# Kernel optimization log

Hardware: AMD Instinct MI355X
Metric: run time of the kernel (lower is better)

Reference implementation:

```python
import jax, jax.numpy as jnp
import numpy as np

EPS_LN = 1e-5
EPS_BN = 1e-5
NUM_HEADS = 8


def _gelu(x):
    return jax.nn.gelu(x, approximate=False)


def _ln(x, w, b):
    # LayerNorm over last (channel) dim, eps=1e-5 (torch default)
    mu = jnp.mean(x, axis=-1, keepdims=True)
    var = jnp.mean((x - mu) ** 2, axis=-1, keepdims=True)
    return (x - mu) / jnp.sqrt(var + EPS_LN) * w + b


def _bn(x, g, b):
    # eval-mode BatchNorm2d on NCHW with running_mean=0, running_var=1
    scale = g * (1.0 + EPS_BN) ** -0.5
    return x * scale[None, :, None, None] + b[None, :, None, None]


def _conv1x1(x, w):
    # x: [B,C,H,W], w: [O,C]
    return jnp.einsum('bchw,oc->bohw', x, w)


def _unfold3(x, r):
    # nn.Unfold(kernel=3, dilation=r, padding=r): gather 3x3 dilated neighborhoods
    B, C, H, W = x.shape
    xp = jnp.pad(x, ((0, 0), (0, 0), (r, r), (r, r)))
    pats = [xp[:, :, i * r:i * r + H, j * r:j * r + W] for i in range(3) for j in range(3)]
    return jnp.stack(pats, axis=2)  # [B,C,9,H,W]


def _atrous_attn(q, k, v, num_heads, r):
    # per-pixel local attention: q [B,C,H,W] attends to 9 dilated neighbors of k/v
    B, C, H, W = q.shape
    hd = C // num_heads
    scale = hd ** -0.5
    qh = q.reshape(B, num_heads, hd, H, W)
    kp = _unfold3(k, r).reshape(B, num_heads, hd, 9, H, W)
    attn = jax.nn.softmax(jnp.einsum('bnchw,bnckhw->bnkhw', qh, kp) * scale, axis=2)
    vp = _unfold3(v, r).reshape(B, num_heads, hd, 9, H, W)
    out = jnp.einsum('bnkhw,bnckhw->bnchw', attn, vp)
    return out.reshape(B, C, H, W).transpose(0, 2, 3, 1)  # [B,H,W,C]


def _window_attn(x_bhwc, qkv_w, proj_w, proj_b, num_heads, r):
    xc = x_bhwc.transpose(0, 3, 1, 2)
    C = xc.shape[1]
    qkv = _conv1x1(xc, qkv_w)  # [B,3C,H,W], order q|k|v
    out = _atrous_attn(qkv[:, :C], qkv[:, C:2 * C], qkv[:, 2 * C:], num_heads, r)
    return jnp.einsum('bhwc,oc->bhwo', out, proj_w) + proj_b


def _mlp(x_bhwc, c1_w, c1_b, bn1_g, bn1_b, dw_w, dw_b, bn2_g, bn2_b, c2_w, c2_b, bn3_g, bn3_b):
    xc = x_bhwc.transpose(0, 3, 1, 2)
    h = _bn(_gelu(_conv1x1(xc, c1_w) + c1_b[None, :, None, None]), bn1_g, bn1_b)
    dw = jax.lax.conv_general_dilated(h, dw_w, (1, 1), 'SAME',
                                      feature_group_count=h.shape[1],
                                      dimension_numbers=('NCHW', 'OIHW', 'NCHW'))
    dw = dw + dw_b[None, :, None, None]
    h = _bn(_gelu(dw + h), bn2_g, bn2_b)
    out = _bn(_conv1x1(h, c2_w) + c2_b[None, :, None, None], bn3_g, bn3_b)
    return out.transpose(0, 2, 3, 1)


def reference(x, ln1_w, ln1_b, ln2_w, ln2_b,
              qkv1_w, proj1_w, proj1_b, qkv2_w, proj2_w, proj2_b, qkv3_w, proj3_w, proj3_b,
              tc_conv_w, tc_conv_b, tc_bn1_g, tc_bn1_b, tc_pool_w, tc_bn2_g, tc_bn2_b,
              tc_trans_w, tc_trans_b, tc_bn3_g, tc_bn3_b,
              mlp_c1_w, mlp_c1_b, mlp_bn1_g, mlp_bn1_b, mlp_dw_w, mlp_dw_b,
              mlp_bn2_g, mlp_bn2_b, mlp_c2_w, mlp_c2_b, mlp_bn3_g, mlp_bn3_b):
    tx = x.transpose(0, 2, 3, 1)  # [B,H,W,C]
    n1 = _ln(tx, ln1_w, ln1_b)
    t1 = tx + _window_attn(n1, qkv1_w, proj1_w, proj1_b, NUM_HEADS, 1)
    t2 = tx + _window_attn(n1, qkv2_w, proj2_w, proj2_b, NUM_HEADS, 2)
    t3 = tx + _window_attn(n1, qkv3_w, proj3_w, proj3_b, NUM_HEADS, 3)
    # Trans_conv: ASPP-style fusion
    xc1 = jax.nn.relu(_bn(_conv1x1(x, tc_conv_w) + tc_conv_b[None, :, None, None], tc_bn1_g, tc_bn1_b))
    pool = jnp.mean(x, axis=(2, 3), keepdims=True)
    pool = jax.nn.relu(_bn(_conv1x1(pool, tc_pool_w), tc_bn2_g, tc_bn2_b))
    pool = jnp.broadcast_to(pool, x.shape)  # bilinear upsample of a 1x1 map == broadcast
    cat = jnp.concatenate([xc1, t1.transpose(0, 3, 1, 2), t2.transpose(0, 3, 1, 2),
                           t3.transpose(0, 3, 1, 2), pool], axis=1)  # [B,5C,H,W]
    tr = jax.nn.relu(_bn(_conv1x1(cat, tc_trans_w) + tc_trans_b[None, :, None, None],
                         tc_bn3_g, tc_bn3_b)).transpose(0, 2, 3, 1)  # [B,H,W,C]
    tr = tr + _mlp(_ln(tr, ln2_w, ln2_b), mlp_c1_w, mlp_c1_b, mlp_bn1_g, mlp_bn1_b,
                   mlp_dw_w, mlp_dw_b, mlp_bn2_g, mlp_bn2_b, mlp_c2_w, mlp_c2_b,
                   mlp_bn3_g, mlp_bn3_b)
    return tr.transpose(0, 3, 1, 2)  # [B,C,H,W]


def setup_inputs():
    key = jax.random.key(0)
    B, C, H, W = 4, 256, 64, 64
    HID = 4 * C
    ks = iter(jax.random.split(key, 64))

    def nrm(shape, scale=0.02):
        return jax.random.normal(next(ks), shape, dtype=jnp.float32) * scale

    inp = {
        'x': jax.random.normal(next(ks), (B, C, H, W), dtype=jnp.float32),
        'ln1_w': jnp.ones((C,), jnp.float32), 'ln1_b': jnp.zeros((C,), jnp.float32),
        'ln2_w': jnp.ones((C,), jnp.float32), 'ln2_b': jnp.zeros((C,), jnp.float32),
    }
    for i in (1, 2, 3):
        inp[f'qkv{i}_w'] = nrm((3 * C, C))
        inp[f'proj{i}_w'] = nrm((C, C))
        inp[f'proj{i}_b'] = jnp.zeros((C,), jnp.float32)
    inp.update(
        tc_conv_w=nrm((C, C)), tc_conv_b=jnp.zeros((C,), jnp.float32),
        tc_bn1_g=jnp.ones((C,), jnp.float32), tc_bn1_b=jnp.zeros((C,), jnp.float32),
        tc_pool_w=nrm((C, C)),
        tc_bn2_g=jnp.ones((C,), jnp.float32), tc_bn2_b=jnp.zeros((C,), jnp.float32),
        tc_trans_w=nrm((C, 5 * C)), tc_trans_b=jnp.zeros((C,), jnp.float32),
        tc_bn3_g=jnp.ones((C,), jnp.float32), tc_bn3_b=jnp.zeros((C,), jnp.float32),
        mlp_c1_w=nrm((HID, C)), mlp_c1_b=jnp.zeros((HID,), jnp.float32),
        mlp_bn1_g=jnp.ones((HID,), jnp.float32), mlp_bn1_b=jnp.zeros((HID,), jnp.float32),
        mlp_dw_w=nrm((HID, 1, 3, 3), 0.1), mlp_dw_b=jnp.zeros((HID,), jnp.float32),
        mlp_bn2_g=jnp.ones((HID,), jnp.float32), mlp_bn2_b=jnp.zeros((HID,), jnp.float32),
        mlp_c2_w=nrm((C, HID)), mlp_c2_b=jnp.zeros((C,), jnp.float32),
        mlp_bn3_g=jnp.ones((C,), jnp.float32), mlp_bn3_b=jnp.zeros((C,), jnp.float32),
    )
    return inp
```

## Files before the change

kernel.cpp:

```cpp
#include <hip/hip_runtime.h>

#define N_PIX 16384
#define CDIM  256
#define HIDD  1024
#define BNS   0.9999950000374997f

typedef __attribute__((ext_vector_type(8))) short  short8;
typedef __attribute__((ext_vector_type(4))) float  f32x4;
typedef __attribute__((ext_vector_type(4))) int    int4v;
typedef __attribute__((ext_vector_type(2))) int    int2v;

__device__ __forceinline__ float b2f(unsigned short u){
  unsigned int x = ((unsigned int)u) << 16; float f;
  __builtin_memcpy(&f, &x, 4); return f;
}
__device__ __forceinline__ unsigned short f2b(float f){
  unsigned int x; __builtin_memcpy(&x, &f, 4);
  unsigned int r = (x + 0x7fffu + ((x >> 16) & 1u)) >> 16;
  return (unsigned short)r;
}
__device__ __forceinline__ float geluf(float x){
  return 0.5f * x * (1.0f + erff(x * 0.70710678118654752f));
}

typedef const __attribute__((address_space(1))) unsigned int* gas_t;
typedef __attribute__((address_space(3))) unsigned int*       las_t;
__device__ __forceinline__ void gload16(const void* g, void* l){
  __builtin_amdgcn_global_load_lds((gas_t)g, (las_t)l, 16, 0, 0);
}

__global__ __launch_bounds__(256) void k_cvt_all(
    const float* __restrict__ s0, const float* __restrict__ s1, const float* __restrict__ s2,
    const float* __restrict__ s3, const float* __restrict__ s4, const float* __restrict__ s5,
    const float* __restrict__ s6, const float* __restrict__ s7, const float* __restrict__ s8,
    const float* __restrict__ s9, unsigned short* __restrict__ wb){
  const float* srcs[10] = {s0,s1,s2,s3,s4,s5,s6,s7,s8,s9};
  const int n[10]   = {196608,196608,196608,65536,65536,65536,65536,327680,262144,262144};
  const int off[10] = {0,196608,393216,589824,655360,720896,786432,851968,1179648,1441792};
  int seg = blockIdx.y;
  int i = (blockIdx.x * 256 + threadIdx.x) * 8;
  if (i >= n[seg]) return;
  const float* src = srcs[seg];
  unsigned short* dst = wb + off[seg];
  f32x4 a = *(const f32x4*)(src + i);
  f32x4 b = *(const f32x4*)(src + i + 4);
  unsigned short o[8];
  #pragma unroll
  for (int j = 0; j < 4; ++j){ o[j] = f2b(a[j]); o[4 + j] = f2b(b[j]); }
  *(int4v*)(dst + i) = *(int4v*)o;
}

__global__ __launch_bounds__(256) void k_dwwT(const float* __restrict__ dww,
                                              unsigned short* __restrict__ dwwT,
                                              float* __restrict__ pm){
  int i = blockIdx.x * 256 + threadIdx.x;
  if (i < 1024) pm[i] = 0.0f;
  if (i >= 9216) return;
  int kk = i >> 10, c = i & 1023;
  dwwT[i] = f2b(dww[c * 9 + kk]);
}

__global__ __launch_bounds__(256) void k_transpose(const float* __restrict__ x,
                                                   unsigned short* __restrict__ xpm,
                                                   float* __restrict__ xpm32,
                                                   float* __restrict__ pm){
  __shared__ __align__(16) float tile[64][65];
  int b = blockIdx.z, c0 = blockIdx.y * 64, p0 = blockIdx.x * 64;
  int t = threadIdx.x;
  int r = t >> 3, k = t & 7;
  float psum[2];
  for (int s = 0; s < 2; ++s){
    int rr = r + s * 32;
    const float* src = x + (((size_t)(b * CDIM + c0 + rr)) << 12) + p0 + k * 8;
    f32x4 a = *(const f32x4*)src;
    f32x4 c = *(const f32x4*)(src + 4);
    psum[s] = a[0] + a[1] + a[2] + a[3] + c[0] + c[1] + c[2] + c[3];
    #pragma unroll
    for (int j = 0; j < 4; ++j){ tile[rr][k * 8 + j] = a[j]; tile[rr][k * 8 + 4 + j] = c[j]; }
  }
  #pragma unroll
  for (int s = 0; s < 2; ++s){
    float v = psum[s];
    v += __shfl_xor(v, 1); v += __shfl_xor(v, 2); v += __shfl_xor(v, 4);
    if ((t & 7) == 0) atomicAdd(&pm[b * 256 + c0 + r + s * 32], v);
  }
  __syncthreads();
  for (int s = 0; s < 2; ++s){
    int pr = r + s * 32;
    float tf[8];
    unsigned short tb[8];
    #pragma unroll
    for (int j = 0; j < 8; ++j){ tf[j] = tile[k * 8 + j][pr]; tb[j] = f2b(tf[j]); }
    size_t rowoff = ((size_t)(b * 4096 + p0 + pr)) << 8;
    *(int4v*)(xpm + rowoff + c0 + k * 8) = *(int4v*)tb;
    *(f32x4*)(xpm32 + rowoff + c0 + k * 8)     = *(f32x4*)&tf[0];
    *(f32x4*)(xpm32 + rowoff + c0 + k * 8 + 4) = *(f32x4*)&tf[4];
  }
}

template<typename IT>
__global__ __launch_bounds__(256) void k_ln(const IT* __restrict__ in,
    const float* __restrict__ w, const float* __restrict__ bia,
    unsigned short* __restrict__ out){
  int row  = blockIdx.x * 4 + (threadIdx.x >> 6);
  int lane = threadIdx.x & 63;
  float v[4];
  const IT* p = in + (size_t)row * CDIM + lane * 4;
  if constexpr (sizeof(IT) == 2){
    int2v d = *(const int2v*)p;
    unsigned short tmp[4]; __builtin_memcpy(tmp, &d, 8);
    #pragma unroll
    for (int j = 0; j < 4; ++j) v[j] = b2f(tmp[j]);
  } else {
    f32x4 d = *(const f32x4*)p;
    #pragma unroll
    for (int j = 0; j < 4; ++j) v[j] = d[j];
  }
  float s  = v[0] + v[1] + v[2] + v[3];
  float s2 = v[0]*v[0] + v[1]*v[1] + v[2]*v[2] + v[3]*v[3];
  #pragma unroll
  for (int m = 1; m < 64; m <<= 1){
    s  += __shfl_xor(s,  m);
    s2 += __shfl_xor(s2, m);
  }
  float mu   = s * (1.0f / 256.0f);
  float var  = s2 * (1.0f / 256.0f) - mu * mu;
  float rstd = rsqrtf(var + 1e-5f);
  unsigned short o[4];
  #pragma unroll
  for (int j = 0; j < 4; ++j){
    int c = lane * 4 + j;
    o[j] = f2b((v[j] - mu) * rstd * w[c] + bia[c]);
  }
  *(int2v*)(out + (size_t)row * CDIM + lane * 4) = *(int2v*)o;
}

template<int MODE, int BM>
__global__ __launch_bounds__(256) void k_gemm(
    const unsigned short* __restrict__ A, const unsigned short* __restrict__ Bw,
    int K, int Nout, int ldb, void* __restrict__ outp,
    const float* __restrict__ bias,
    const float* __restrict__ bng,
    const float* __restrict__ bnb,
    const float* __restrict__ auxf,
    int catoff)
{
  constexpr int NI = BM / 32;
  __shared__ __align__(16) unsigned short As[2][BM * 32];
  __shared__ __align__(16) unsigned short Bs[2][128 * 32];
  int t = threadIdx.x;
  int m0 = blockIdx.y * BM, n0 = blockIdx.x * 128;
  int lane = t & 63;
  int w  = __builtin_amdgcn_readfirstlane(t >> 6);
  int wm = w >> 1, wn = w & 1;
  int lr = lane & 15, kb = lane >> 4;
  const bool doA = (w * 16 < BM);

  f32x4 acc[NI][4];
  f32x4 z = {0.f, 0.f, 0.f, 0.f};
  #pragma unroll
  for (int i = 0; i < NI; ++i)
    #pragma unroll
    for (int j = 0; j < 4; ++j) acc[i][j] = z;

  int srow = lane >> 2, schunk = (lane & 3) * 8;
  const unsigned short* gA  = A  + (size_t)(m0 + w * 16 + srow) * K   + schunk;
  const unsigned short* gB0 = Bw + (size_t)(n0 + w * 16 + srow) * ldb + schunk;
  const unsigned short* gB1 = Bw + (size_t)(n0 + 64 + w * 16 + srow) * ldb + schunk;

  const int nt = K >> 5;
  if (doA) gload16(gA, As[0] + w * 512);
  gload16(gB0, Bs[0] + w * 512);
  gload16(gB1, Bs[0] + 2048 + w * 512);
  __syncthreads();

  for (int tt = 0; tt < nt; ++tt){
    int cur = tt & 1;
    if (tt + 1 < nt){
      int k1 = (tt + 1) << 5;
      if (doA) gload16(gA + k1, As[cur ^ 1] + w * 512);
      gload16(gB0 + k1, Bs[cur ^ 1] + w * 512);
      gload16(gB1 + k1, Bs[cur ^ 1] + 2048 + w * 512);
    }
    short8 af[NI], bf_[4];
    #pragma unroll
    for (int i = 0; i < NI; ++i)
      af [i] = *(const short8*)&As[cur][(wm * (BM / 2) + i * 16 + lr) * 32 + kb * 8];
    #pragma unroll
    for (int j = 0; j < 4; ++j)
      bf_[j] = *(const short8*)&Bs[cur][(wn * 64 + j * 16 + lr) * 32 + kb * 8];
    #pragma unroll
    for (int i = 0; i < NI; ++i)
      #pragma unroll
      for (int j = 0; j < 4; ++j)
        acc[i][j] = __builtin_amdgcn_mfma_f32_16x16x32_bf16(af[i], bf_[j], acc[i][j], 0, 0, 0);
    __syncthreads();
  }

  #pragma unroll
  for (int i = 0; i < NI; ++i){
    int rowb = m0 + wm * (BM / 2) + i * 16 + kb * 4;
    #pragma unroll
    for (int j = 0; j < 4; ++j){
      int col = n0 + wn * 64 + j * 16 + lr;
      #pragma unroll
      for (int rr = 0; rr < 4; ++rr){
        int row = rowb + rr;
        float v = acc[i][j][rr];
        if constexpr (MODE == 0){
          ((unsigned short*)outp)[(size_t)row * Nout + col] = f2b(v);
        } else if constexpr (MODE == 3){
          v += bias[col] + auxf[((row >> 12) << 8) + col];
          v = v * (bng[col] * BNS) + bnb[col];
          v = fmaxf(v, 0.0f);
          ((float*)outp)[(size_t)row * CDIM + col] = v;
        } else if constexpr (MODE == 4){
          v = geluf(v + bias[col]);
          v = v * (bng[col] * BNS) + bnb[col];
          ((unsigned short*)outp)[(size_t)row * HIDD + col] = f2b(v);
        } else {
          v = (v + bias[col]) * (bng[col] * BNS) + bnb[col];
          v += auxf[(size_t)row * CDIM + col];
          int b = row >> 12, hw = row & 4095;
          ((float*)outp)[(((size_t)(b * CDIM + col)) << 12) + hw] = v;
        }
      }
    }
  }
}

struct GrpArgs {
  const unsigned short* A[4];
  const unsigned short* B[4];
  const float* bias[4];
  int lda[4];
  int catoff[4];
};

__global__ __launch_bounds__(256) void k_gemm_grp(GrpArgs ga,
    const float* __restrict__ xpm32, const float* __restrict__ bng,
    const float* __restrict__ bnb, unsigned short* __restrict__ CAT)
{
  __shared__ __align__(16) unsigned short As[2][64 * 32];
  __shared__ __align__(16) unsigned short Bs[2][128 * 32];
  int t = threadIdx.x;
  int g  = blockIdx.x >> 1;
  int n0 = (blockIdx.x & 1) * 128;
  int m0 = blockIdx.y * 64;
  const unsigned short* A  = ga.A[g];
  const unsigned short* Bw = ga.B[g];
  const float* bias = ga.bias[g];
  int lda = ga.lda[g];
  int catoff = ga.catoff[g];

  int lane = t & 63;
  int w  = __builtin_amdgcn_readfirstlane(t >> 6);
  int wm = w >> 1, wn = w & 1;
  int lr = lane & 15, kb = lane >> 4;

  f32x4 acc[2][4];
  f32x4 z = {0.f, 0.f, 0.f, 0.f};
  #pragma unroll
  for (int i = 0; i < 2; ++i)
    #pragma unroll
    for (int j = 0; j < 4; ++j) acc[i][j] = z;

  int srow = lane >> 2, schunk = (lane & 3) * 8;
  const unsigned short* gA  = A  + (size_t)(m0 + w * 16 + srow) * lda + schunk;
  const unsigned short* gB0 = Bw + (size_t)(n0 + w * 16 + srow) * 256 + schunk;
  const unsigned short* gB1 = Bw + (size_t)(n0 + 64 + w * 16 + srow) * 256 + schunk;

  gload16(gA,  As[0] + w * 512);
  gload16(gB0, Bs[0] + w * 512);
  gload16(gB1, Bs[0] + 2048 + w * 512);
  __syncthreads();

  for (int tt = 0; tt < 8; ++tt){
    int cur = tt & 1;
    if (tt + 1 < 8){
      int k1 = (tt + 1) << 5;
      gload16(gA  + k1, As[cur ^ 1] + w * 512);
      gload16(gB0 + k1, Bs[cur ^ 1] + w * 512);
      gload16(gB1 + k1, Bs[cur ^ 1] + 2048 + w * 512);
    }
    short8 af[2], bf_[4];
    #pragma unroll
    for (int i = 0; i < 2; ++i)
      af [i] = *(const short8*)&As[cur][(wm * 32 + i * 16 + lr) * 32 + kb * 8];
    #pragma unroll
    for (int j = 0; j < 4; ++j)
      bf_[j] = *(const short8*)&Bs[cur][(wn * 64 + j * 16 + lr) * 32 + kb * 8];
    #pragma unroll
    for (int i = 0; i < 2; ++i)
      #pragma unroll
      for (int j = 0; j < 4; ++j)
        acc[i][j] = __builtin_amdgcn_mfma_f32_16x16x32_bf16(af[i], bf_[j], acc[i][j], 0, 0, 0);
    __syncthreads();
  }

  #pragma unroll
  for (int i = 0; i < 2; ++i){
    int rowb = m0 + wm * 32 + i * 16 + kb * 4;
    #pragma unroll
    for (int j = 0; j < 4; ++j){
      int col = n0 + wn * 64 + j * 16 + lr;
      #pragma unroll
      for (int rr = 0; rr < 4; ++rr){
        int row = rowb + rr;
        float v = acc[i][j][rr];
        if (g == 3){
          v = (v + bias[col]) * (bng[col] * BNS) + bnb[col];
          v = fmaxf(v, 0.0f);
        } else {
          v += bias[col] + xpm32[(size_t)row * CDIM + col];
        }
        CAT[(size_t)row * HIDD + catoff + col] = f2b(v);
      }
    }
  }
}

__global__ __launch_bounds__(256) void k_attn3(const unsigned short* __restrict__ QKV3,
                                               unsigned short* __restrict__ F3){
  int grp = blockIdx.x >> 10;
  int r = grp + 1;
  int t = (blockIdx.x & 1023) * 256 + threadIdx.x;
  int half = t & 1, head = (t >> 1) & 7, pix = t >> 4;
  int hw = pix & 4095, h = hw >> 6, w = hw & 63;
  const unsigned short* base = QKV3 + (size_t)pix * 2304 + grp * 768 + head * 32 + half * 16;

  float q[16];
  #pragma unroll
  for (int c8 = 0; c8 < 2; ++c8){
    int4v d = *(const int4v*)(base + c8 * 8);
    unsigned short tmp[8]; __builtin_memcpy(tmp, &d, 16);
    #pragma unroll
    for (int j = 0; j < 8; ++j) q[c8 * 8 + j] = b2f(tmp[j]);
  }
  float logit[9];
  #pragma unroll
  for (int jj = 0; jj < 9; ++jj){
    int dh = (jj / 3 - 1) * r, dw = (jj % 3 - 1) * r;
    int hh = h + dh, ww = w + dw;
    float d = 0.0f;
    if (hh >= 0 && hh < 64 && ww >= 0 && ww < 64){
      const unsigned short* kr = base + (dh * 64 + dw) * 2304 + 256;
      #pragma unroll
      for (int c8 = 0; c8 < 2; ++c8){
        int4v dd = *(const int4v*)(kr + c8 * 8);
        unsigned short tmp[8]; __builtin_memcpy(tmp, &dd, 16);
        #pragma unroll
        for (int j = 0; j < 8; ++j) d += q[c8 * 8 + j] * b2f(tmp[j]);
      }
    }
    d += __shfl_xor(d, 1);
    logit[jj] = d * 0.17677669529663687f;
  }
  float m = logit[0];
  #pragma unroll
  for (int jj = 1; jj < 9; ++jj) m = fmaxf(m, logit[jj]);
  float p[9], s = 0.0f;
  #pragma unroll
  for (int jj = 0; jj < 9; ++jj){ p[jj] = __expf(logit[jj] - m); s += p[jj]; }
  float inv = 1.0f / s;
  float o[16];
  #pragma unroll
  for (int j = 0; j < 16; ++j) o[j] = 0.0f;
  #pragma unroll
  for (int jj = 0; jj < 9; ++jj){
    int dh = (jj / 3 - 1) * r, dw = (jj % 3 - 1) * r;
    int hh = h + dh, ww = w + dw;
    if (hh >= 0 && hh < 64 && ww >= 0 && ww < 64){
      float pj = p[jj] * inv;
      const unsigned short* vr = base + (dh * 64 + dw) * 2304 + 512;
      #pragma unroll
      for (int c8 = 0; c8 < 2; ++c8){
        int4v dd = *(const int4v*)(vr + c8 * 8);
        unsigned short tmp[8]; __builtin_memcpy(tmp, &dd, 16);
        #pragma unroll
        for (int j = 0; j < 8; ++j) o[c8 * 8 + j] += pj * b2f(tmp[j]);
      }
    }
  }
  unsigned short ob[16];
  #pragma unroll
  for (int j = 0; j < 16; ++j) ob[j] = f2b(o[j]);
  unsigned short* op = F3 + (size_t)pix * 768 + grp * 256 + head * 32 + half * 16;
  *(int4v*)(op)     = *(int4v*)&ob[0];
  *(int4v*)(op + 8) = *(int4v*)&ob[8];
}

__global__ __launch_bounds__(256) void k_dwconv(const unsigned short* __restrict__ H,
    const unsigned short* __restrict__ dwwT, const float* __restrict__ dwb,
    const float* __restrict__ g, const float* __restrict__ bb,
    unsigned short* __restrict__ H2){
  int t = blockIdx.x * 256 + threadIdx.x;
  int chunk = t & 127, pix = t >> 7;
  int hw = pix & 4095, h = hw >> 6, w = hw & 63;
  int c0 = chunk * 8;
  float acc[8], hc[8];
  {
    int4v dd = *(const int4v*)(H + (size_t)pix * HIDD + c0);
    unsigned short tmp[8]; __builtin_memcpy(tmp, &dd, 16);
    #pragma unroll
    for (int j = 0; j < 8; ++j){ hc[j] = b2f(tmp[j]); acc[j] = 0.0f; }
  }
  #pragma unroll
  for (int di = -1; di <= 1; ++di)
    #pragma unroll
    for (int dj = -1; dj <= 1; ++dj){
      int hh = h + di, ww = w + dj;
      if (hh < 0 || hh >= 64 || ww < 0 || ww >= 64) continue;
      int kk = (di + 1) * 3 + (dj + 1);
      int4v dd = *(const int4v*)(H + ((size_t)(pix + di * 64 + dj)) * HIDD + c0);
      int4v wv = *(const int4v*)(dwwT + kk * 1024 + c0);
      unsigned short tmp[8], wt[8];
      __builtin_memcpy(tmp, &dd, 16);
      __builtin_memcpy(wt,  &wv, 16);
      #pragma unroll
      for (int j = 0; j < 8; ++j) acc[j] += b2f(wt[j]) * b2f(tmp[j]);
    }
  f32x4 bv0 = *(const f32x4*)(dwb + c0), bv1 = *(const f32x4*)(dwb + c0 + 4);
  f32x4 gv0 = *(const f32x4*)(g   + c0), gv1 = *(const f32x4*)(g   + c0 + 4);
  f32x4 cv0 = *(const f32x4*)(bb  + c0), cv1 = *(const f32x4*)(bb  + c0 + 4);
  float bvv[8], gvv[8], cvv[8];
  #pragma unroll
  for (int j = 0; j < 4; ++j){
    bvv[j] = bv0[j]; bvv[4 + j] = bv1[j];
    gvv[j] = gv0[j]; gvv[4 + j] = gv1[j];
    cvv[j] = cv0[j]; cvv[4 + j] = cv1[j];
  }
  unsigned short ob[8];
  #pragma unroll
  for (int j = 0; j < 8; ++j){
    float v = acc[j] + bvv[j] + hc[j];
    v = geluf(v);
    v = v * (gvv[j] * BNS) + cvv[j];
    ob[j] = f2b(v);
  }
  *(int4v*)(H2 + (size_t)pix * HIDD + c0) = *(int4v*)ob;
}

__global__ __launch_bounds__(256) void k_poolfb(const float* __restrict__ pm,
    const float* __restrict__ pw, const float* __restrict__ g,
    const float* __restrict__ bb, const float* __restrict__ tw,
    float* __restrict__ pb){
  int b = blockIdx.x, o = threadIdx.x;
  __shared__ float v[256];
  __shared__ float pfs[256];
  v[o] = pm[b * 256 + o] * (1.0f / 4096.0f);
  __syncthreads();
  float acc = 0.0f;
  const float* wr = pw + (size_t)o * 256;
  for (int c = 0; c < 256; ++c) acc += v[c] * wr[c];
  float val = acc * (g[o] * BNS) + bb[o];
  pfs[o] = fmaxf(val, 0.0f);
  __syncthreads();
  float acc2 = 0.0f;
  const float* tr = tw + (size_t)o * 1280 + 1024;
  for (int c = 0; c < 256; ++c) acc2 += pfs[c] * tr[c];
  pb[b * 256 + o] = acc2;
}

extern "C" void kernel_launch(void* const* d_in, const int* in_sizes, int n_in,
                              void* d_out, int out_size, void* d_ws, size_t ws_size,
                              hipStream_t stream){
  const float* x     = (const float*)d_in[0];
  const float* ln1w  = (const float*)d_in[1];
  const float* ln1b  = (const float*)d_in[2];
  const float* ln2w  = (const float*)d_in[3];
  const float* ln2b  = (const float*)d_in[4];
  const float* qkvw[3]  = {(const float*)d_in[5], (const float*)d_in[8],  (const float*)d_in[11]};
  const float* projw[3] = {(const float*)d_in[6], (const float*)d_in[9],  (const float*)d_in[12]};
  const float* projb[3] = {(const float*)d_in[7], (const float*)d_in[10], (const float*)d_in[13]};
  const float* tcw   = (const float*)d_in[14];
  const float* tcb   = (const float*)d_in[15];
  const float* bn1g  = (const float*)d_in[16];
  const float* bn1b  = (const float*)d_in[17];
  const float* poolw = (const float*)d_in[18];
  const float* bn2g  = (const float*)d_in[19];
  const float* bn2b  = (const float*)d_in[20];
  const float* trw   = (const float*)d_in[21];
  const float* trb   = (const float*)d_in[22];
  const float* bn3g  = (const float*)d_in[23];
  const float* bn3b  = (const float*)d_in[24];
  const float* c1w   = (const float*)d_in[25];
  const float* c1b   = (const float*)d_in[26];
  const float* mbn1g = (const float*)d_in[27];
  const float* mbn1b = (const float*)d_in[28];
  const float* dww   = (const float*)d_in[29];
  const float* dwb   = (const float*)d_in[30];
  const float* mbn2g = (const float*)d_in[31];
  const float* mbn2b = (const float*)d_in[32];
  const float* c2w   = (const float*)d_in[33];
  const float* c2b   = (const float*)d_in[34];
  const float* mbn3g = (const float*)d_in[35];
  const float* mbn3b = (const float*)d_in[36];

  char* ws = (char*)d_ws;
  unsigned short* Xpm = (unsigned short*)(ws);
  unsigned short* N1  = (unsigned short*)(ws + 8388608);
  unsigned short* CAT = (unsigned short*)(ws + 16777216);
  float*          TR  = (float*)        (ws + 50331648);
  float*          Xpm32 = TR;
  unsigned short* H   = (unsigned short*)(ws + 67108864);
  unsigned short* H2  = (unsigned short*)(ws + 100663296);
  unsigned short* Wb  = (unsigned short*)(ws + 134217728);
  unsigned short* projbw[3] = {Wb + 589824, Wb + 655360, Wb + 720896};
  unsigned short* tcwb  = Wb + 786432;
  unsigned short* trwb  = Wb + 851968;
  unsigned short* c1wb  = Wb + 1179648;
  unsigned short* c2wb  = Wb + 1441792;
  unsigned short* dwwT  = Wb + 1703936;
  float*          pm  = (float*)(ws + 134217728 + 3428352);
  float*          pb  = pm + 1024;
  unsigned short* E3  = (unsigned short*)(ws + 140509184);
  unsigned short* F3  = (unsigned short*)(ws + 216006656);

  k_cvt_all<<<dim3(160, 10), 256, 0, stream>>>(qkvw[0], qkvw[1], qkvw[2],
                                               projw[0], projw[1], projw[2],
                                               tcw, trw, c1w, c2w, Wb);
  k_dwwT<<<36, 256, 0, stream>>>(dww, dwwT, pm);
  k_transpose<<<dim3(64, 4, 4), 256, 0, stream>>>(x, Xpm, Xpm32, pm);
  k_ln<unsigned short><<<4096, 256, 0, stream>>>(Xpm, ln1w, ln1b, N1);
  k_poolfb<<<4, 256, 0, stream>>>(pm, poolw, bn2g, bn2b, trw, pb);

  k_gemm<0, 64><<<dim3(18, 256), 256, 0, stream>>>(N1, Wb, 256, 2304, 256, E3,
                                                   nullptr, nullptr, nullptr, nullptr, 0);
  k_attn3<<<3072, 256, 0, stream>>>(E3, F3);
  {
    GrpArgs ga;
    ga.A[0] = F3;       ga.A[1] = F3 + 256; ga.A[2] = F3 + 512; ga.A[3] = Xpm;
    ga.B[0] = projbw[0]; ga.B[1] = projbw[1]; ga.B[2] = projbw[2]; ga.B[3] = tcwb;
    ga.bias[0] = projb[0]; ga.bias[1] = projb[1]; ga.bias[2] = projb[2]; ga.bias[3] = tcb;
    ga.lda[0] = 768; ga.lda[1] = 768; ga.lda[2] = 768; ga.lda[3] = 256;
    ga.catoff[0] = 256; ga.catoff[1] = 512; ga.catoff[2] = 768; ga.catoff[3] = 0;
    k_gemm_grp<<<dim3(8, 256), 256, 0, stream>>>(ga, Xpm32, bn1g, bn1b, CAT);
  }
  k_gemm<3, 32><<<dim3(2, 512), 256, 0, stream>>>(CAT, trwb, 1024, 256, 1280, TR,
                                                  trb, bn3g, bn3b, pb, 0);
  k_ln<float><<<4096, 256, 0, stream>>>(TR, ln2w, ln2b, N1);
  k_gemm<4, 64><<<dim3(8, 256), 256, 0, stream>>>(N1, c1wb, 256, 1024, 256, H,
                                                  c1b, mbn1g, mbn1b, nullptr, 0);
  k_dwconv<<<8192, 256, 0, stream>>>(H, dwwT, dwb, mbn2g, mbn2b, H2);
  k_gemm<5, 32><<<dim3(2, 512), 256, 0, stream>>>(H2, c2wb, 1024, 256, 1024, d_out,
                                                  c2b, mbn3g, mbn3b, TR, 0);
}
```

Measured before the change: 402.2 us.

## Swizzle GEMM LDS tiles and use partial vmcnt waits for prefetch overlap

The two bf16 MFMA GEMM kernels now XOR-swizzle the 16-byte k-chunk position in the shared-memory A/B tiles, applying it both to the global-to-LDS load addresses and to the fragment reads, so LDS bank conflicts are reduced. The full __syncthreads at the top of each k-step is replaced by s_waitcnt vmcnt(N) plus a raw s_barrier, so the prefetch of the next tile can stay in flight while the current tile is consumed. The hand-written waitcnt counts depend on exactly how many loads gload16 issues, and if that assumption is wrong the kernel can read stale data.

```diff
diff --git a/kernel.cpp b/kernel.cpp
--- a/kernel.cpp
+++ b/kernel.cpp
@@ -163,16 +163,17 @@
     #pragma unroll
     for (int j = 0; j < 4; ++j) acc[i][j] = z;
 
-  int srow = lane >> 2, schunk = (lane & 3) * 8;
+  int srow = lane >> 2;
+  int schunk = (((lane & 3) ^ ((lane >> 3) & 3))) * 8;
   const unsigned short* gA  = A  + (size_t)(m0 + w * 16 + srow) * K   + schunk;
   const unsigned short* gB0 = Bw + (size_t)(n0 + w * 16 + srow) * ldb + schunk;
   const unsigned short* gB1 = Bw + (size_t)(n0 + 64 + w * 16 + srow) * ldb + schunk;
+  int kbx = (kb ^ ((lr >> 1) & 3)) * 8;
 
   const int nt = K >> 5;
   if (doA) gload16(gA, As[0] + w * 512);
   gload16(gB0, Bs[0] + w * 512);
   gload16(gB1, Bs[0] + 2048 + w * 512);
-  __syncthreads();
 
   for (int tt = 0; tt < nt; ++tt){
     int cur = tt & 1;
@@ -181,20 +182,27 @@
       if (doA) gload16(gA + k1, As[cur ^ 1] + w * 512);
       gload16(gB0 + k1, Bs[cur ^ 1] + w * 512);
       gload16(gB1 + k1, Bs[cur ^ 1] + 2048 + w * 512);
-    }
+      if (doA) asm volatile("s_waitcnt vmcnt(3)" ::: "memory");
+      else     asm volatile("s_waitcnt vmcnt(2)" ::: "memory");
+    } else {
+      asm volatile("s_waitcnt vmcnt(0)" ::: "memory");
+    }
+    __builtin_amdgcn_s_barrier();
     short8 af[NI], bf_[4];
     #pragma unroll
     for (int i = 0; i < NI; ++i)
-      af [i] = *(const short8*)&As[cur][(wm * (BM / 2) + i * 16 + lr) * 32 + kb * 8];
+      af [i] = *(const short8*)&As[cur][(wm * (BM / 2) + i * 16 + lr) * 32 + kbx];
     #pragma unroll
     for (int j = 0; j < 4; ++j)
-      bf_[j] = *(const short8*)&Bs[cur][(wn * 64 + j * 16 + lr) * 32 + kb * 8];
+      bf_[j] = *(const short8*)&Bs[cur][(wn * 64 + j * 16 + lr) * 32 + kbx];
     #pragma unroll
     for (int i = 0; i < NI; ++i)
       #pragma unroll
       for (int j = 0; j < 4; ++j)
         acc[i][j] = __builtin_amdgcn_mfma_f32_16x16x32_bf16(af[i], bf_[j], acc[i][j], 0, 0, 0);
-    __syncthreads();
+    asm volatile("s_waitcnt lgkmcnt(0)" ::: "memory");
+    __builtin_amdgcn_sched_barrier(0);
+    __builtin_amdgcn_s_barrier();
   }
 
   #pragma unroll
@@ -265,15 +273,16 @@
     #pragma unroll
     for (int j = 0; j < 4; ++j) acc[i][j] = z;
 
-  int srow = lane >> 2, schunk = (lane & 3) * 8;
+  int srow = lane >> 2;
+  int schunk = (((lane & 3) ^ ((lane >> 3) & 3))) * 8;
   const unsigned short* gA  = A  + (size_t)(m0 + w * 16 + srow) * lda + schunk;
   const unsigned short* gB0 = Bw + (size_t)(n0 + w * 16 + srow) * 256 + schunk;
   const unsigned short* gB1 = Bw + (size_t)(n0 + 64 + w * 16 + srow) * 256 + schunk;
+  int kbx = (kb ^ ((lr >> 1) & 3)) * 8;
 
   gload16(gA,  As[0] + w * 512);
   gload16(gB0, Bs[0] + w * 512);
   gload16(gB1, Bs[0] + 2048 + w * 512);
-  __syncthreads();
 
   for (int tt = 0; tt < 8; ++tt){
     int cur = tt & 1;
@@ -282,20 +291,26 @@
       gload16(gA  + k1, As[cur ^ 1] + w * 512);
       gload16(gB0 + k1, Bs[cur ^ 1] + w * 512);
       gload16(gB1 + k1, Bs[cur ^ 1] + 2048 + w * 512);
-    }
+      asm volatile("s_waitcnt vmcnt(3)" ::: "memory");
+    } else {
+      asm volatile("s_waitcnt vmcnt(0)" ::: "memory");
+    }
+    __builtin_amdgcn_s_barrier();
     short8 af[2], bf_[4];
     #pragma unroll
     for (int i = 0; i < 2; ++i)
-      af [i] = *(const short8*)&As[cur][(wm * 32 + i * 16 + lr) * 32 + kb * 8];
+      af [i] = *(const short8*)&As[cur][(wm * 32 + i * 16 + lr) * 32 + kbx];
     #pragma unroll
     for (int j = 0; j < 4; ++j)
-      bf_[j] = *(const short8*)&Bs[cur][(wn * 64 + j * 16 + lr) * 32 + kb * 8];
+      bf_[j] = *(const short8*)&Bs[cur][(wn * 64 + j * 16 + lr) * 32 + kbx];
     #pragma unroll
     for (int i = 0; i < 2; ++i)
       #pragma unroll
       for (int j = 0; j < 4; ++j)
         acc[i][j] = __builtin_amdgcn_mfma_f32_16x16x32_bf16(af[i], bf_[j], acc[i][j], 0, 0, 0);
-    __syncthreads();
+    asm volatile("s_waitcnt lgkmcnt(0)" ::: "memory");
+    __builtin_amdgcn_sched_barrier(0);
+    __builtin_amdgcn_s_barrier();
   }
 
   #pragma unroll
```

New measurement: 398.3 us. About the same (-1.0%).
